# Kernel optimization log

Hardware: AMD Instinct MI355X
Metric: run time of the kernel (lower is better)

Reference implementation:

```python
import jax, jax.numpy as jnp
import numpy as np

NUM_HEADS = 8
NUM_POINTS = 9


def _bilinear_sample(img, gx, gy):
    """grid_sample, mode=bilinear, padding=zeros, align_corners=True.
    img: (B, C, H, W); gx, gy: (B, M) pixel coords. Returns (B, C, M)."""
    Bc, C, H, W = img.shape
    imgf = img.reshape(Bc, C, H * W)
    x0 = jnp.floor(gx)
    y0 = jnp.floor(gy)
    wx1 = gx - x0
    wy1 = gy - y0

    def corner(xi, yi, w):
        valid = (xi >= 0) & (xi < W) & (yi >= 0) & (yi < H)
        xi_c = jnp.clip(xi, 0, W - 1).astype(jnp.int32)
        yi_c = jnp.clip(yi, 0, H - 1).astype(jnp.int32)
        idx = yi_c * W + xi_c  # (B, M)
        g = jax.vmap(lambda im, ix: im[:, ix])(imgf, idx)  # (B, C, M)
        return g * (w * valid)[:, None, :]

    return (corner(x0, y0, (1 - wx1) * (1 - wy1))
            + corner(x0 + 1, y0, wx1 * (1 - wy1))
            + corner(x0, y0 + 1, (1 - wx1) * wy1)
            + corner(x0 + 1, y0 + 1, wx1 * wy1))


def setup_inputs() -> dict:
    key = jax.random.key(0)
    ks = jax.random.split(key, 6)
    B, Hp, Wp, T, D = 4, 64, 64, 3, 256
    N = Hp * Wp
    Hh, P = NUM_HEADS, NUM_POINTS
    x = jax.random.normal(ks[0], (B, N, T, D), dtype=jnp.float32)
    # offset/attn projections: small random (orig inits them to 0, which is degenerate for testing)
    W_off = jax.random.normal(ks[1], (D, Hh * P * 2), dtype=jnp.float32) * 0.01
    b_off = jnp.zeros((Hh * P * 2,), dtype=jnp.float32)
    W_attn = jax.random.normal(ks[2], (D, Hh * P), dtype=jnp.float32) * 0.01
    b_attn = jnp.zeros((Hh * P,), dtype=jnp.float32)
    W_v = jax.random.normal(ks[3], (D, D), dtype=jnp.float32) * 0.02
    b_v = jnp.zeros((D,), dtype=jnp.float32)
    W_o = jax.random.normal(ks[4], (D, D), dtype=jnp.float32) * 0.02
    b_o = jnp.zeros((D,), dtype=jnp.float32)
    return {"x": x, "W_off": W_off, "b_off": b_off, "W_attn": W_attn,
            "b_attn": b_attn, "W_v": W_v, "b_v": b_v, "W_o": W_o,
            "b_o": b_o, "Hp": Hp, "Wp": Wp}


def reference(x, W_off, b_off, W_attn, b_attn, W_v, b_v, W_o, b_o, Hp, Wp):
    B, N, T, D = x.shape
    Hh, P = NUM_HEADS, NUM_POINTS
    dh = D // Hh

    query = x[:, :, T // 2]  # (B, N, D) middle frame
    offset = (query @ W_off + b_off).reshape(B, N, Hh, P, 2)
    attn = jax.nn.softmax((query @ W_attn + b_attn).reshape(B, N, Hh, P), axis=-1)

    # reference points in [-1, 1], xy order (x = width coord)
    gh, gw = jnp.meshgrid(jnp.arange(Hp, dtype=jnp.float32),
                          jnp.arange(Wp, dtype=jnp.float32), indexing='ij')
    ref = jnp.stack([gw, gh], axis=-1).reshape(N, 2)
    ref = ref / jnp.asarray([Wp - 1, Hp - 1], dtype=jnp.float32) * 2 - 1

    loc = ref[None, :, None, None, :] + offset  # (B, N, H, P, 2) normalized

    value = (x @ W_v + b_v).reshape(B, N, T, Hh, dh)
    # (B, H, T, dh, N) -> (B*H*T, dh, Hp, Wp)
    val = jnp.transpose(value, (0, 3, 2, 4, 1)).reshape(B * Hh * T, dh, Hp, Wp)

    # per-(b,h) grid, shared across frames; fold T into batch of the sampler
    grid = jnp.transpose(loc, (0, 2, 1, 3, 4))  # (B, H, N, P, 2)
    grid = jnp.broadcast_to(grid[:, :, None], (B, Hh, T, N, P, 2))
    grid = grid.reshape(B * Hh * T, N * P, 2)
    gx = (grid[..., 0] + 1) * 0.5 * (Wp - 1)
    gy = (grid[..., 1] + 1) * 0.5 * (Hp - 1)

    sampled = _bilinear_sample(val, gx, gy)  # (B*H*T, dh, N*P)
    sampled = sampled.reshape(B, Hh, T, dh, N, P)

    # weighted sum over points, summed over frames
    out = jnp.einsum('bhtdnp,bnhp->bnhd', sampled, attn).reshape(B, N, D)
    return out @ W_o + b_o
```

## Files before the change

### kernel.cpp

```cpp
#include <hip/hip_runtime.h>
#include <hip/hip_bf16.h>


#define NH_ 8
#define DH_ 32
#define MM_ 16384

typedef __attribute__((ext_vector_type(8))) short bf16x8;
typedef __attribute__((ext_vector_type(4))) short bf16x4;
typedef __attribute__((ext_vector_type(4))) float f32x4;

static __device__ __forceinline__ unsigned short f2bf(float f) {
  unsigned int u = __float_as_uint(f);
  u = (u + 0x7fff + ((u >> 16) & 1)) >> 16;
  return (unsigned short)u;
}
static __device__ __forceinline__ float bf2f(unsigned short h) {
  return __uint_as_float(((unsigned int)h) << 16);
}
static __device__ __forceinline__ void split8(const float4 f0, const float4 f1,
                                              bf16x8& hv, bf16x8& lv) {
  float vv[8] = {f0.x, f0.y, f0.z, f0.w, f1.x, f1.y, f1.z, f1.w};
#pragma unroll
  for (int j = 0; j < 8; ++j) {
    unsigned short h = f2bf(vv[j]);
    hv[j] = (short)h;
    lv[j] = (short)f2bf(vv[j] - bf2f(h));
  }
}

__global__ __launch_bounds__(256) void prep(
    const float* __restrict__ x,
    const float* __restrict__ W_off, const float* __restrict__ W_attn,
    const float* __restrict__ W_v, const float* __restrict__ W_o,
    const float* __restrict__ b_off, const float* __restrict__ b_attn,
    unsigned short* __restrict__ ash, unsigned short* __restrict__ asl,
    unsigned short* __restrict__ xmh, unsigned short* __restrict__ xml,
    unsigned short* __restrict__ wvh, unsigned short* __restrict__ wvl,
    unsigned short* __restrict__ wch, unsigned short* __restrict__ wcl,
    unsigned short* __restrict__ woh, unsigned short* __restrict__ wol,
    float* __restrict__ bcat) {
  const int bid = blockIdx.x, t = threadIdx.x;
  if (bid < 4096) {
    const int gid = bid * 256 + t;
    const int row = gid >> 6, c4 = (gid & 63) * 4;
    const float* xr = x + (size_t)row * 768 + c4;
    float4 a0 = *(const float4*)xr;
    float4 a1 = *(const float4*)(xr + 256);
    float4 a2 = *(const float4*)(xr + 512);
    float s[4] = {a0.x + a1.x + a2.x, a0.y + a1.y + a2.y,
                  a0.z + a1.z + a2.z, a0.w + a1.w + a2.w};
    float m[4] = {a1.x, a1.y, a1.z, a1.w};
    bf16x4 shv, slv, mhv, mlv;
#pragma unroll
    for (int j = 0; j < 4; ++j) {
      unsigned short h = f2bf(s[j]);
      shv[j] = (short)h; slv[j] = (short)f2bf(s[j] - bf2f(h));
      unsigned short h2 = f2bf(m[j]);
      mhv[j] = (short)h2; mlv[j] = (short)f2bf(m[j] - bf2f(h2));
    }
    const size_t o = (size_t)row * 256 + c4;
    *(bf16x4*)(ash + o) = shv;  *(bf16x4*)(asl + o) = slv;
    *(bf16x4*)(xmh + o) = mhv;  *(bf16x4*)(xml + o) = mlv;
  } else {
    const int n = bid - 4096;
    {
      float v = W_v[(size_t)t * 256 + n];
      unsigned short h = f2bf(v);
      wvh[n * 256 + t] = h; wvl[n * 256 + t] = f2bf(v - bf2f(h));
    }
    {
      float v = W_o[(size_t)t * 256 + n];
      unsigned short h = f2bf(v);
      woh[n * 256 + t] = h; wol[n * 256 + t] = f2bf(v - bf2f(h));
    }
    if (n < 216) {
      float v = (n < 144) ? W_off[(size_t)t * 144 + n] : W_attn[(size_t)t * 72 + (n - 144)];
      unsigned short h = f2bf(v);
      wch[n * 256 + t] = h; wcl[n * 256 + t] = f2bf(v - bf2f(h));
    }
    if (n == 0 && t < 216) bcat[t] = (t < 144) ? b_off[t] : b_attn[t - 144];
  }
}

__global__ __launch_bounds__(256, 4) void mgemm01(
    const unsigned short* __restrict__ Ahi, const unsigned short* __restrict__ Alo,
    const unsigned short* __restrict__ Xmh, const unsigned short* __restrict__ Xml,
    const unsigned short* __restrict__ Wvh, const unsigned short* __restrict__ Wvl,
    const unsigned short* __restrict__ Wch, const unsigned short* __restrict__ Wcl,
    const float* __restrict__ b_v, const float* __restrict__ bcat,
    float* __restrict__ valsum, float* __restrict__ proj) {
  __shared__ unsigned short Ah[64][64], Al[64][64], Bh[64][64], Bl[64][64];
  const int mode1 = blockIdx.y >= 4;
  const int n0 = (blockIdx.y & 3) * 64;
  const int m0 = blockIdx.x * 64;
  const int tid = threadIdx.x, wid = tid >> 6, lane = tid & 63;
  const int am = (wid >> 1) * 32, bn = (wid & 1) * 32;
  const int fr = lane & 15, kg = lane >> 4;
  const unsigned short* Ahs = mode1 ? Xmh : Ahi;
  const unsigned short* Als = mode1 ? Xml : Alo;
  const unsigned short* Bhs = mode1 ? Wch : Wvh;
  const unsigned short* Bls = mode1 ? Wcl : Wvl;

  const int r0s = tid >> 3, c0s = tid & 7;
  const int r1s = r0s + 32;
  const int d0s = r0s * 64 + ((c0s ^ (r0s & 7)) * 8);
  const int d1s = r1s * 64 + ((c0s ^ (r1s & 7)) * 8);

  f32x4 acc[2][2];
#pragma unroll
  for (int i = 0; i < 2; ++i)
#pragma unroll
    for (int j = 0; j < 2; ++j) acc[i][j] = (f32x4)(0.f);

  bf16x8 pah[2], pal[2], pbh[2], pbl[2];

#define LOADT01(k0)                                                          \
  {                                                                          \
    size_t a0 = (size_t)(m0 + r0s) * 256 + (k0) + c0s * 8;                   \
    size_t a1 = (size_t)(m0 + r1s) * 256 + (k0) + c0s * 8;                   \
    pah[0] = *(const bf16x8*)(Ahs + a0); pal[0] = *(const bf16x8*)(Als + a0);\
    pah[1] = *(const bf16x8*)(Ahs + a1); pal[1] = *(const bf16x8*)(Als + a1);\
    int nr0 = n0 + r0s, nr1 = n0 + r1s;                                      \
    size_t b0 = (size_t)nr0 * 256 + (k0) + c0s * 8;                          \
    size_t b1 = (size_t)nr1 * 256 + (k0) + c0s * 8;                          \
    if (!mode1 || nr0 < 216) {                                               \
      pbh[0] = *(const bf16x8*)(Bhs + b0); pbl[0] = *(const bf16x8*)(Bls + b0);\
    } else { pbh[0] = (bf16x8)(short)0; pbl[0] = (bf16x8)(short)0; }         \
    if (!mode1 || nr1 < 216) {                                               \
      pbh[1] = *(const bf16x8*)(Bhs + b1); pbl[1] = *(const bf16x8*)(Bls + b1);\
    } else { pbh[1] = (bf16x8)(short)0; pbl[1] = (bf16x8)(short)0; }         \
  }

#define WRITET()                                                             \
  {                                                                          \
    *(bf16x8*)(&Ah[0][0] + d0s) = pah[0]; *(bf16x8*)(&Al[0][0] + d0s) = pal[0];\
    *(bf16x8*)(&Ah[0][0] + d1s) = pah[1]; *(bf16x8*)(&Al[0][0] + d1s) = pal[1];\
    *(bf16x8*)(&Bh[0][0] + d0s) = pbh[0]; *(bf16x8*)(&Bl[0][0] + d0s) = pbl[0];\
    *(bf16x8*)(&Bh[0][0] + d1s) = pbh[1]; *(bf16x8*)(&Bl[0][0] + d1s) = pbl[1];\
  }

#define COMPUTET()                                                           \
  _Pragma("unroll")                                                          \
  for (int ks = 0; ks < 2; ++ks) {                                           \
    const int kc = ks * 4 + kg;                                              \
    bf16x8 ah[2], al[2], bh[2], bl[2];                                       \
    _Pragma("unroll")                                                        \
    for (int mi = 0; mi < 2; ++mi) {                                         \
      int m = am + mi * 16 + fr;                                             \
      int o = m * 64 + ((kc ^ (m & 7)) * 8);                                 \
      ah[mi] = *(const bf16x8*)(&Ah[0][0] + o);                              \
      al[mi] = *(const bf16x8*)(&Al[0][0] + o);                              \
    }                                                                        \
    _Pragma("unroll")                                                        \
    for (int ni = 0; ni < 2; ++ni) {                                         \
      int nn = bn + ni * 16 + fr;                                            \
      int o = nn * 64 + ((kc ^ (nn & 7)) * 8);                               \
      bh[ni] = *(const bf16x8*)(&Bh[0][0] + o);                              \
      bl[ni] = *(const bf16x8*)(&Bl[0][0] + o);                              \
    }                                                                        \
    _Pragma("unroll")                                                        \
    for (int mi = 0; mi < 2; ++mi)                                           \
      _Pragma("unroll")                                                      \
      for (int ni = 0; ni < 2; ++ni) {                                       \
        acc[mi][ni] = __builtin_amdgcn_mfma_f32_16x16x32_bf16(ah[mi], bh[ni], acc[mi][ni], 0, 0, 0);\
        acc[mi][ni] = __builtin_amdgcn_mfma_f32_16x16x32_bf16(ah[mi], bl[ni], acc[mi][ni], 0, 0, 0);\
        acc[mi][ni] = __builtin_amdgcn_mfma_f32_16x16x32_bf16(al[mi], bh[ni], acc[mi][ni], 0, 0, 0);\
      }                                                                      \
  }

  LOADT01(0);
  WRITET();
  __syncthreads();
#pragma unroll
  for (int t = 0; t < 4; ++t) {
    if (t < 3) LOADT01((t + 1) * 64);
    COMPUTET();
    __syncthreads();
    if (t < 3) { WRITET(); __syncthreads(); }
  }

  const int ro = kg * 4;
#pragma unroll
  for (int mi = 0; mi < 2; ++mi)
#pragma unroll
    for (int ni = 0; ni < 2; ++ni) {
      int col = n0 + bn + ni * 16 + fr;
      if (mode1 && col >= 216) continue;
      int rowb = m0 + am + mi * 16 + ro;
      float bv = mode1 ? bcat[col] : b_v[col] * 3.f;
#pragma unroll
      for (int r = 0; r < 4; ++r) {
        int grow = rowb + r;
        float v = acc[mi][ni][r] + bv;
        if (mode1) {
          proj[(size_t)grow * 216 + col] = v;
        } else {
          int b = grow >> 12, nn2 = grow & 4095;
          int h = col >> 5, d = col & 31;
          valsum[(((size_t)(b * NH_ + h) << 12) + nn2) * DH_ + d] = v;
        }
      }
    }
#undef LOADT01
#undef WRITET
#undef COMPUTET
}

__global__ __launch_bounds__(256, 4) void mgemm2(
    const float* __restrict__ Af, 
    const unsigned short* __restrict__ Bhs, const unsigned short* __restrict__ Bls,
    const float* __restrict__ bias, float* __restrict__ Cout) {
  __shared__ unsigned short Ah[64][64], Al[64][64], Bh[64][64], Bl[64][64];
  const int n0 = blockIdx.y * 64;
  const int m0 = blockIdx.x * 64;
  const int tid = threadIdx.x, wid = tid >> 6, lane = tid & 63;
  const int am = (wid >> 1) * 32, bn = (wid & 1) * 32;
  const int fr = lane & 15, kg = lane >> 4;

  const int r0s = tid >> 3, c0s = tid & 7;
  const int r1s = r0s + 32;
  const int d0s = r0s * 64 + ((c0s ^ (r0s & 7)) * 8);
  const int d1s = r1s * 64 + ((c0s ^ (r1s & 7)) * 8);

  f32x4 acc[2][2];
#pragma unroll
  for (int i = 0; i < 2; ++i)
#pragma unroll
    for (int j = 0; j < 2; ++j) acc[i][j] = (f32x4)(0.f);

  float4 pf[2][2];
  bf16x8 pbh[2], pbl[2];

#define LOADT2(k0)                                                           \
  {                                                                          \
    const float* s0 = Af + (size_t)(m0 + r0s) * 256 + (k0) + c0s * 8;        \
    const float* s1 = Af + (size_t)(m0 + r1s) * 256 + (k0) + c0s * 8;        \
    pf[0][0] = *(const float4*)s0; pf[0][1] = *(const float4*)(s0 + 4);      \
    pf[1][0] = *(const float4*)s1; pf[1][1] = *(const float4*)(s1 + 4);      \
    size_t b0 = (size_t)(n0 + r0s) * 256 + (k0) + c0s * 8;                   \
    size_t b1 = (size_t)(n0 + r1s) * 256 + (k0) + c0s * 8;                   \
    pbh[0] = *(const bf16x8*)(Bhs + b0); pbl[0] = *(const bf16x8*)(Bls + b0);\
    pbh[1] = *(const bf16x8*)(Bhs + b1); pbl[1] = *(const bf16x8*)(Bls + b1);\
  }

#define WRITET2()                                                            \
  {                                                                          \
    bf16x8 hv, lv;                                                           \
    split8(pf[0][0], pf[0][1], hv, lv);                                      \
    *(bf16x8*)(&Ah[0][0] + d0s) = hv; *(bf16x8*)(&Al[0][0] + d0s) = lv;      \
    split8(pf[1][0], pf[1][1], hv, lv);                                      \
    *(bf16x8*)(&Ah[0][0] + d1s) = hv; *(bf16x8*)(&Al[0][0] + d1s) = lv;      \
    *(bf16x8*)(&Bh[0][0] + d0s) = pbh[0]; *(bf16x8*)(&Bl[0][0] + d0s) = pbl[0];\
    *(bf16x8*)(&Bh[0][0] + d1s) = pbh[1]; *(bf16x8*)(&Bl[0][0] + d1s) = pbl[1];\
  }

#define COMPUTET2()                                                          \
  _Pragma("unroll")                                                          \
  for (int ks = 0; ks < 2; ++ks) {                                           \
    const int kc = ks * 4 + kg;                                              \
    bf16x8 ah[2], al[2], bh[2], bl[2];                                       \
    _Pragma("unroll")                                                        \
    for (int mi = 0; mi < 2; ++mi) {                                         \
      int m = am + mi * 16 + fr;                                             \
      int o = m * 64 + ((kc ^ (m & 7)) * 8);                                 \
      ah[mi] = *(const bf16x8*)(&Ah[0][0] + o);                              \
      al[mi] = *(const bf16x8*)(&Al[0][0] + o);                              \
    }                                                                        \
    _Pragma("unroll")                                                        \
    for (int ni = 0; ni < 2; ++ni) {                                         \
      int nn = bn + ni * 16 + fr;                                            \
      int o = nn * 64 + ((kc ^ (nn & 7)) * 8);                               \
      bh[ni] = *(const bf16x8*)(&Bh[0][0] + o);                              \
      bl[ni] = *(const bf16x8*)(&Bl[0][0] + o);                              \
    }                                                                        \
    _Pragma("unroll")                                                        \
    for (int mi = 0; mi < 2; ++mi)                                           \
      _Pragma("unroll")                                                      \
      for (int ni = 0; ni < 2; ++ni) {                                       \
        acc[mi][ni] = __builtin_amdgcn_mfma_f32_16x16x32_bf16(ah[mi], bh[ni], acc[mi][ni], 0, 0, 0);\
        acc[mi][ni] = __builtin_amdgcn_mfma_f32_16x16x32_bf16(ah[mi], bl[ni], acc[mi][ni], 0, 0, 0);\
        acc[mi][ni] = __builtin_amdgcn_mfma_f32_16x16x32_bf16(al[mi], bh[ni], acc[mi][ni], 0, 0, 0);\
      }                                                                      \
  }

  LOADT2(0);
  WRITET2();
  __syncthreads();
#pragma unroll
  for (int t = 0; t < 4; ++t) {
    if (t < 3) LOADT2((t + 1) * 64);
    COMPUTET2();
    __syncthreads();
    if (t < 3) { WRITET2(); __syncthreads(); }
  }

  const int ro = kg * 4;
#pragma unroll
  for (int mi = 0; mi < 2; ++mi)
#pragma unroll
    for (int ni = 0; ni < 2; ++ni) {
      int col = n0 + bn + ni * 16 + fr;
      int rowb = m0 + am + mi * 16 + ro;
      float bv = bias[col];
#pragma unroll
      for (int r = 0; r < 4; ++r)
        Cout[(size_t)(rowb + r) * 256 + col] = acc[mi][ni][r] + bv;
    }
#undef LOADT2
#undef WRITET2
#undef COMPUTET2
}

struct IW { int idx; float w; };

__global__ __launch_bounds__(256) void sample4(const float* __restrict__ valsum,
                                               const float* __restrict__ proj,
                                               float* __restrict__ inter) {
  const int bid = blockIdx.x;
  const int wv = threadIdx.x >> 6;
  const int lane = threadIdx.x & 63;
  const int row = ((bid & 7) << 11) + ((bid >> 3) << 2) + wv;
  const int b = row >> 12, n = row & 4095;

  __shared__ IW cwi[4][72][4];
  __shared__ float sap[4][76];

  const float* pr = proj + (size_t)row * 216;
  if (lane < 8) {
    const float* pa = pr + 144 + lane * 9;
    float lg[9], mx = -1e30f;
#pragma unroll
    for (int p = 0; p < 9; ++p) { lg[p] = pa[p]; mx = fmaxf(mx, lg[p]); }
    float s = 0.f;
#pragma unroll
    for (int p = 0; p < 9; ++p) { lg[p] = __expf(lg[p] - mx); s += lg[p]; }
    float inv = 1.f / s;
#pragma unroll
    for (int p = 0; p < 9; ++p) sap[wv][lane * 9 + p] = lg[p] * inv;
  }
  __syncthreads();
  for (int e = lane; e < 72; e += 64) {
    float ox = pr[e * 2], oy = pr[e * 2 + 1];
    float gx = (float)(n & 63) + ox * 31.5f;
    float gy = (float)(n >> 6) + oy * 31.5f;
    float fx0 = floorf(gx), fy0 = floorf(gy);
    float wx1 = gx - fx0, wy1 = gy - fy0;
    float wx0 = 1.f - wx1, wy0 = 1.f - wy1;
    int x0 = (int)fx0, y0 = (int)fy0, x1 = x0 + 1, y1 = y0 + 1;
    bool vx0 = (x0 >= 0) & (x0 < 64), vx1 = (x1 >= 0) & (x1 < 64);
    bool vy0 = (y0 >= 0) & (y0 < 64), vy1 = (y1 >= 0) & (y1 < 64);
    int x0c = min(max(x0, 0), 63), x1c = min(max(x1, 0), 63);
    int y0c = min(max(y0, 0), 63), y1c = min(max(y1, 0), 63);
    const float a = sap[wv][e];
    cwi[wv][e][0] = IW{(y0c * 64 + x0c) * DH_, (vx0 & vy0) ? wx0 * wy0 * a : 0.f};
    cwi[wv][e][1] = IW{(y0c * 64 + x1c) * DH_, (vx1 & vy0) ? wx1 * wy0 * a : 0.f};
    cwi[wv][e][2] = IW{(y1c * 64 + x0c) * DH_, (vx0 & vy1) ? wx0 * wy1 * a : 0.f};
    cwi[wv][e][3] = IW{(y1c * 64 + x1c) * DH_, (vx1 & vy1) ? wx1 * wy1 * a : 0.f};
  }
  __syncthreads();

  const int h = lane >> 3, d4 = (lane & 7) * 4;
  const float* vb = valsum + (((size_t)(b * NH_ + h)) << 12) * DH_ + d4;
  float ax = 0.f, ay = 0.f, az = 0.f, aw = 0.f;
#pragma unroll
  for (int pb = 0; pb < 9; pb += 3) {
    float4 v[12]; float w[12];
#pragma unroll
    for (int q = 0; q < 3; ++q) {
      const int hp = h * 9 + pb + q;
#pragma unroll
      for (int c = 0; c < 4; ++c) {
        IW e = cwi[wv][hp][c];
        v[q * 4 + c] = *(const float4*)(vb + e.idx);
        w[q * 4 + c] = e.w;
      }
    }
#pragma unroll
    for (int j = 0; j < 12; ++j) {
      ax += w[j] * v[j].x; ay += w[j] * v[j].y;
      az += w[j] * v[j].z; aw += w[j] * v[j].w;
    }
  }
  *(float4*)(inter + (size_t)row * 256 + h * DH_ + d4) = make_float4(ax, ay, az, aw);
}

extern "C" void kernel_launch(void* const* d_in, const int* in_sizes, int n_in,
                              void* d_out, int out_size, void* d_ws, size_t ws_size,
                              hipStream_t stream) {
  const float* x      = (const float*)d_in[0];
  const float* W_off  = (const float*)d_in[1];
  const float* b_off  = (const float*)d_in[2];
  const float* W_attn = (const float*)d_in[3];
  const float* b_attn = (const float*)d_in[4];
  const float* W_v    = (const float*)d_in[5];
  const float* b_v    = (const float*)d_in[6];
  const float* W_o    = (const float*)d_in[7];
  const float* b_o    = (const float*)d_in[8];
  float* out = (float*)d_out;

  float* valsum = (float*)d_ws;
  float* proj   = valsum + (size_t)MM_ * 256;
  float* bcat   = proj + (size_t)MM_ * 216;
  unsigned short* ash = (unsigned short*)(bcat + 256);
  unsigned short* asl = ash + (size_t)MM_ * 256;
  unsigned short* xmh = asl + (size_t)MM_ * 256;
  unsigned short* xml = xmh + (size_t)MM_ * 256;
  unsigned short* wvh = xml + (size_t)MM_ * 256;
  unsigned short* wvl = wvh + 65536;
  unsigned short* wch = wvl + 65536;
  unsigned short* wcl = wch + 55296;
  unsigned short* woh = wcl + 55296;
  unsigned short* wol = woh + 65536;
  float* inter = (float*)ash;

  prep<<<dim3(4352), dim3(256), 0, stream>>>(x, W_off, W_attn, W_v, W_o, b_off, b_attn,
                                             ash, asl, xmh, xml,
                                             wvh, wvl, wch, wcl, woh, wol, bcat);
  mgemm01<<<dim3(256, 8), dim3(256), 0, stream>>>(ash, asl, xmh, xml, wvh, wvl, wch, wcl,
                                                  b_v, bcat, valsum, proj);
  sample4<<<dim3(4096), dim3(256), 0, stream>>>(valsum, proj, inter);
  mgemm2<<<dim3(256, 4), dim3(256), 0, stream>>>(inter, woh, wol, b_o, out);
}
```

Baseline: 166.3 us.

## Store value tensor in fp16 and pre-split sampler output to bf16 hi/lo

The value projection (valsum) is now stored as fp16 instead of fp32, which halves the bytes read by the random-gather sampler. The sampler now writes its output already split into bf16 hi/lo pairs, so the output GEMM loads them directly and no longer converts from fp32 per tile. Storing values in fp16 adds rounding error to the sampled values and could lower accuracy against the fp32 reference.

After: 162.2 us. 1.02x faster.

```diff
diff --git a/kernel.cpp b/kernel.cpp
--- a/kernel.cpp
+++ b/kernel.cpp
@@ -1,5 +1,6 @@
 #include <hip/hip_runtime.h>
 #include <hip/hip_bf16.h>
+#include <hip/hip_fp16.h>
 
 
 #define NH_ 8
@@ -17,16 +18,6 @@
 }
 static __device__ __forceinline__ float bf2f(unsigned short h) {
   return __uint_as_float(((unsigned int)h) << 16);
-}
-static __device__ __forceinline__ void split8(const float4 f0, const float4 f1,
-                                              bf16x8& hv, bf16x8& lv) {
-  float vv[8] = {f0.x, f0.y, f0.z, f0.w, f1.x, f1.y, f1.z, f1.w};
-#pragma unroll
-  for (int j = 0; j < 8; ++j) {
-    unsigned short h = f2bf(vv[j]);
-    hv[j] = (short)h;
-    lv[j] = (short)f2bf(vv[j] - bf2f(h));
-  }
 }
 
 __global__ __launch_bounds__(256) void prep(
@@ -89,7 +80,7 @@
     const unsigned short* __restrict__ Wvh, const unsigned short* __restrict__ Wvl,
     const unsigned short* __restrict__ Wch, const unsigned short* __restrict__ Wcl,
     const float* __restrict__ b_v, const float* __restrict__ bcat,
-    float* __restrict__ valsum, float* __restrict__ proj) {
+    __half* __restrict__ valsum, float* __restrict__ proj) {
   __shared__ unsigned short Ah[64][64], Al[64][64], Bh[64][64], Bl[64][64];
   const int mode1 = blockIdx.y >= 4;
   const int n0 = (blockIdx.y & 3) * 64;
@@ -198,7 +189,7 @@
         } else {
           int b = grow >> 12, nn2 = grow & 4095;
           int h = col >> 5, d = col & 31;
-          valsum[(((size_t)(b * NH_ + h) << 12) + nn2) * DH_ + d] = v;
+          valsum[(((size_t)(b * NH_ + h) << 12) + nn2) * DH_ + d] = __float2half_rn(v);
         }
       }
     }
@@ -208,7 +199,7 @@
 }
 
 __global__ __launch_bounds__(256, 4) void mgemm2(
-    const float* __restrict__ Af, 
+    const unsigned short* __restrict__ Ahi, const unsigned short* __restrict__ Alo,
     const unsigned short* __restrict__ Bhs, const unsigned short* __restrict__ Bls,
     const float* __restrict__ bias, float* __restrict__ Cout) {
   __shared__ unsigned short Ah[64][64], Al[64][64], Bh[64][64], Bl[64][64];
@@ -229,15 +220,14 @@
 #pragma unroll
     for (int j = 0; j < 2; ++j) acc[i][j] = (f32x4)(0.f);
 
-  float4 pf[2][2];
-  bf16x8 pbh[2], pbl[2];
+  bf16x8 pah[2], pal[2], pbh[2], pbl[2];
 
 #define LOADT2(k0)                                                           \
   {                                                                          \
-    const float* s0 = Af + (size_t)(m0 + r0s) * 256 + (k0) + c0s * 8;        \
-    const float* s1 = Af + (size_t)(m0 + r1s) * 256 + (k0) + c0s * 8;        \
-    pf[0][0] = *(const float4*)s0; pf[0][1] = *(const float4*)(s0 + 4);      \
-    pf[1][0] = *(const float4*)s1; pf[1][1] = *(const float4*)(s1 + 4);      \
+    size_t a0 = (size_t)(m0 + r0s) * 256 + (k0) + c0s * 8;                   \
+    size_t a1 = (size_t)(m0 + r1s) * 256 + (k0) + c0s * 8;                   \
+    pah[0] = *(const bf16x8*)(Ahi + a0); pal[0] = *(const bf16x8*)(Alo + a0);\
+    pah[1] = *(const bf16x8*)(Ahi + a1); pal[1] = *(const bf16x8*)(Alo + a1);\
     size_t b0 = (size_t)(n0 + r0s) * 256 + (k0) + c0s * 8;                   \
     size_t b1 = (size_t)(n0 + r1s) * 256 + (k0) + c0s * 8;                   \
     pbh[0] = *(const bf16x8*)(Bhs + b0); pbl[0] = *(const bf16x8*)(Bls + b0);\
@@ -246,11 +236,8 @@
 
 #define WRITET2()                                                            \
   {                                                                          \
-    bf16x8 hv, lv;                                                           \
-    split8(pf[0][0], pf[0][1], hv, lv);                                      \
-    *(bf16x8*)(&Ah[0][0] + d0s) = hv; *(bf16x8*)(&Al[0][0] + d0s) = lv;      \
-    split8(pf[1][0], pf[1][1], hv, lv);                                      \
-    *(bf16x8*)(&Ah[0][0] + d1s) = hv; *(bf16x8*)(&Al[0][0] + d1s) = lv;      \
+    *(bf16x8*)(&Ah[0][0] + d0s) = pah[0]; *(bf16x8*)(&Al[0][0] + d0s) = pal[0];\
+    *(bf16x8*)(&Ah[0][0] + d1s) = pah[1]; *(bf16x8*)(&Al[0][0] + d1s) = pal[1];\
     *(bf16x8*)(&Bh[0][0] + d0s) = pbh[0]; *(bf16x8*)(&Bl[0][0] + d0s) = pbl[0];\
     *(bf16x8*)(&Bh[0][0] + d1s) = pbh[1]; *(bf16x8*)(&Bl[0][0] + d1s) = pbl[1];\
   }
@@ -314,9 +301,10 @@
 
 struct IW { int idx; float w; };
 
-__global__ __launch_bounds__(256) void sample4(const float* __restrict__ valsum,
+__global__ __launch_bounds__(256) void sample4(const __half* __restrict__ valsum,
                                                const float* __restrict__ proj,
-                                               float* __restrict__ inter) {
+                                               unsigned short* __restrict__ ihi,
+                                               unsigned short* __restrict__ ilo) {
   const int bid = blockIdx.x;
   const int wv = threadIdx.x >> 6;
   const int lane = threadIdx.x & 63;
@@ -361,28 +349,40 @@
   __syncthreads();
 
   const int h = lane >> 3, d4 = (lane & 7) * 4;
-  const float* vb = valsum + (((size_t)(b * NH_ + h)) << 12) * DH_ + d4;
+  const __half* vb = valsum + (((size_t)(b * NH_ + h)) << 12) * DH_ + d4;
   float ax = 0.f, ay = 0.f, az = 0.f, aw = 0.f;
 #pragma unroll
   for (int pb = 0; pb < 9; pb += 3) {
-    float4 v[12]; float w[12];
+    float2 v[24]; float w[12];
 #pragma unroll
     for (int q = 0; q < 3; ++q) {
       const int hp = h * 9 + pb + q;
 #pragma unroll
       for (int c = 0; c < 4; ++c) {
         IW e = cwi[wv][hp][c];
-        v[q * 4 + c] = *(const float4*)(vb + e.idx);
+        const __half2* p = (const __half2*)(vb + e.idx);
+        v[(q * 4 + c) * 2 + 0] = __half22float2(p[0]);
+        v[(q * 4 + c) * 2 + 1] = __half22float2(p[1]);
         w[q * 4 + c] = e.w;
       }
     }
 #pragma unroll
     for (int j = 0; j < 12; ++j) {
-      ax += w[j] * v[j].x; ay += w[j] * v[j].y;
-      az += w[j] * v[j].z; aw += w[j] * v[j].w;
-    }
-  }
-  *(float4*)(inter + (size_t)row * 256 + h * DH_ + d4) = make_float4(ax, ay, az, aw);
+      ax += w[j] * v[j * 2].x;     ay += w[j] * v[j * 2].y;
+      az += w[j] * v[j * 2 + 1].x; aw += w[j] * v[j * 2 + 1].y;
+    }
+  }
+  float av[4] = {ax, ay, az, aw};
+  bf16x4 hv, lv;
+#pragma unroll
+  for (int j = 0; j < 4; ++j) {
+    unsigned short hh = f2bf(av[j]);
+    hv[j] = (short)hh;
+    lv[j] = (short)f2bf(av[j] - bf2f(hh));
+  }
+  const size_t o = (size_t)row * 256 + lane * 4;
+  *(bf16x4*)(ihi + o) = hv;
+  *(bf16x4*)(ilo + o) = lv;
 }
 
 extern "C" void kernel_launch(void* const* d_in, const int* in_sizes, int n_in,
@@ -399,9 +399,9 @@
   const float* b_o    = (const float*)d_in[8];
   float* out = (float*)d_out;
 
-  float* valsum = (float*)d_ws;
-  float* proj   = valsum + (size_t)MM_ * 256;
-  float* bcat   = proj + (size_t)MM_ * 216;
+  __half* valsum = (__half*)d_ws;
+  float* proj    = (float*)(valsum + (size_t)MM_ * 256);
+  float* bcat    = proj + (size_t)MM_ * 216;
   unsigned short* ash = (unsigned short*)(bcat + 256);
   unsigned short* asl = ash + (size_t)MM_ * 256;
   unsigned short* xmh = asl + (size_t)MM_ * 256;
@@ -412,13 +412,14 @@
   unsigned short* wcl = wch + 55296;
   unsigned short* woh = wcl + 55296;
   unsigned short* wol = woh + 65536;
-  float* inter = (float*)ash;
+  unsigned short* ihi = ash;
+  unsigned short* ilo = asl;
 
   prep<<<dim3(4352), dim3(256), 0, stream>>>(x, W_off, W_attn, W_v, W_o, b_off, b_attn,
                                              ash, asl, xmh, xml,
                                              wvh, wvl, wch, wcl, woh, wol, bcat);
   mgemm01<<<dim3(256, 8), dim3(256), 0, stream>>>(ash, asl, xmh, xml, wvh, wvl, wch, wcl,
                                                   b_v, bcat, valsum, proj);
-  sample4<<<dim3(4096), dim3(256), 0, stream>>>(valsum, proj, inter);
-  mgemm2<<<dim3(256, 4), dim3(256), 0, stream>>>(inter, woh, wol, b_o, out);
-}
+  sample4<<<dim3(4096), dim3(256), 0, stream>>>(valsum, proj, ihi, ilo);
+  mgemm2<<<dim3(256, 4), dim3(256), 0, stream>>>(ihi, ilo, woh, wol, b_o, out);
+}
```
